# Kernel tuning notes

Measured on AMD Instinct MI355X. Metric: run time of the kernel, lower is better.

The kernel has to match this reference:

```python
import jax, jax.numpy as jnp
import numpy as np

NUM_HEADS = 16


def rotate_half(x):
    half = x.shape[-1] // 2
    return jnp.concatenate((-x[..., half:], x[..., :half]), axis=-1)


def rope_tables(seq_len, head_dim, dtype=jnp.float32):
    inv_freq = 1.0 / (10000.0 ** (jnp.arange(0, head_dim, 2, dtype=jnp.float32) / head_dim))
    t = jnp.arange(seq_len, dtype=jnp.float32)
    freqs = jnp.outer(t, inv_freq)                 # [S, hd/2]
    emb = jnp.concatenate((freqs, freqs), axis=-1)  # [S, hd]
    return jnp.cos(emb).astype(dtype), jnp.sin(emb).astype(dtype)


def setup_inputs() -> dict:
    key = jax.random.key(0)
    k1, k2, k3 = jax.random.split(key, 3)
    B, S, D = 2, 2048, 1024
    x = jax.random.normal(k1, (B, S, D), dtype=jnp.float32)
    # causal lower-triangular mask, broadcast over batch/heads
    mask = jnp.tril(jnp.ones((S, S), dtype=bool))[None, None, :, :]
    w_qkv = jax.random.normal(k2, (3 * D, D), dtype=jnp.float32) * (D ** -0.5)
    w_out = jax.random.normal(k3, (D, D), dtype=jnp.float32) * (D ** -0.5)
    return {"x": x, "mask": mask, "w_qkv": w_qkv, "w_out": w_out}


def reference(x, mask, w_qkv, w_out):
    B, S, D = x.shape
    H = NUM_HEADS
    hd = D // H
    scale = hd ** -0.5

    qkv = jnp.einsum('bsd,ed->bse', x, w_qkv)          # [B, S, 3D]
    q, k, v = jnp.split(qkv, 3, axis=-1)

    def split(t):
        return t.reshape(B, S, H, hd).transpose(0, 2, 1, 3)  # [B, H, S, hd]

    q, k, v = split(q), split(k), split(v)

    cos, sin = rope_tables(S, hd, x.dtype)             # [S, hd]
    cos = cos[None, None]
    sin = sin[None, None]
    q = q * cos + rotate_half(q) * sin
    k = k * cos + rotate_half(k) * sin

    attn = jnp.einsum('bhqd,bhkd->bhqk', q, k) * scale  # [B, H, S, S]
    attn = jnp.where(mask, attn, jnp.float32(-jnp.inf).astype(attn.dtype))
    attn = jax.nn.softmax(attn, axis=-1)
    out = jnp.einsum('bhqk,bhkd->bhqd', attn, v)        # [B, H, S, hd]
    out = out.transpose(0, 2, 1, 3).reshape(B, S, D)
    return jnp.einsum('bsd,ed->bse', out, w_out)
```

## Files before the change

kernel.cpp:

```cpp
#include <hip/hip_runtime.h>
#include <hip/hip_bf16.h>

typedef __attribute__((ext_vector_type(8))) __bf16 bf16x8;
typedef __attribute__((ext_vector_type(4))) __bf16 bf16x4;
typedef __attribute__((ext_vector_type(2))) __bf16 bf16x2;
typedef __attribute__((ext_vector_type(4))) float f32x4;
typedef __attribute__((ext_vector_type(16))) float f32x16;

#define SEQ 2048
#define NH 16
#define HD 64
#define DMODEL 1024
#define BATCH 2
#define MTOT 4096
#define NCH 26

__device__ __forceinline__ void gl_lds16(const void* g, void* l) {
    __builtin_amdgcn_global_load_lds(
        (const __attribute__((address_space(1))) void*)(uintptr_t)g,
        (__attribute__((address_space(3))) void*)(uintptr_t)l,
        16, 0, 0);
}

__device__ __forceinline__ unsigned pk2(float x, float y) {
    union { bf16x2 h; unsigned u; } c;
    c.h = bf16x2{ (__bf16)x, (__bf16)y };
    return c.u;
}

__constant__ int4 FCHUNK[32] = {
    {0,0,1,-1},{1,0,2,-1},{2,0,3,-1},{3,0,4,-1},{4,0,5,-1},{5,0,6,-1},
    {6,0,4,0},{6,4,7,1},{7,0,4,2},{7,4,8,3},
    {8,0,5,4},{8,5,9,5},{9,0,5,6},{9,5,10,7},
    {10,0,6,8},{10,6,11,9},
    {11,0,4,10},{11,4,8,11},{11,8,12,12},
    {12,0,5,13},{12,5,9,14},{12,9,13,15},
    {13,0,5,16},{13,5,10,17},{13,10,14,18},
    {14,0,5,19},{14,5,10,20},{14,10,15,21},
    {15,0,4,22},{15,4,8,23},{15,8,12,24},{15,12,16,25}
};

__global__ __launch_bounds__(256) void cast3(const float4* __restrict__ x,
                                             const float4* __restrict__ wq,
                                             const float4* __restrict__ wo,
                                             __bf16* __restrict__ xb,
                                             __bf16* __restrict__ wqb,
                                             __bf16* __restrict__ wob) {
    const int NX  = 1024 * 1024;
    const int NWQ = 768 * 1024;
    const int NTOT = NX + NWQ + 256 * 1024;
    int i = blockIdx.x * 256 + threadIdx.x;
    if (i >= NTOT) return;
    float4 v; __bf16* dst; int j;
    if (i < NX)            { j = i;            v = x[j];  dst = xb;  }
    else if (i < NX + NWQ) { j = i - NX;       v = wq[j]; dst = wqb; }
    else                   { j = i - NX - NWQ; v = wo[j]; dst = wob; }
    bf16x4 o = { (__bf16)v.x, (__bf16)v.y, (__bf16)v.z, (__bf16)v.w };
    *(bf16x4*)(dst + (size_t)j * 4) = o;
}

__global__ __launch_bounds__(256) void gemm_qkv(const __bf16* __restrict__ A,
                                                const __bf16* __restrict__ Bt,
                                                __bf16* __restrict__ Qp,
                                                __bf16* __restrict__ Kp,
                                                __bf16* __restrict__ Vt) {
    const int K = 1024;
    __shared__ __bf16 sA[128 * 64];
    __shared__ __bf16 sB[128 * 64];
    const int tid = threadIdx.x, lane = tid & 63, wave = tid >> 6;
    const int lrow = lane & 15, quad = lane >> 4;
    const int m0 = blockIdx.y * 128, n0 = blockIdx.x * 128;
    const int wm = wave >> 1, wn = wave & 1;

    const __bf16* ap[4]; const __bf16* bp[4]; int ldso[4];
#pragma unroll
    for (int i = 0; i < 4; ++i) {
        int r0 = i * 32 + wave * 8;
        int row = r0 + (lane >> 3);
        int cg = (lane & 7) ^ (row & 7);
        ap[i] = A + (size_t)(m0 + row) * K + cg * 8;
        bp[i] = Bt + (size_t)(n0 + row) * K + cg * 8;
        ldso[i] = r0 * 128;
    }
    int arow[4], brow[4];
#pragma unroll
    for (int i = 0; i < 4; ++i) {
        arow[i] = wm * 64 + i * 16 + lrow;
        brow[i] = wn * 64 + i * 16 + lrow;
    }

    f32x4 z = {0.f, 0.f, 0.f, 0.f};
    f32x4 acc[4][4];
#pragma unroll
    for (int i = 0; i < 4; ++i)
#pragma unroll
        for (int j = 0; j < 4; ++j) acc[i][j] = z;

    char* sAb = (char*)sA; char* sBb = (char*)sB;
    for (int k0 = 0; k0 < K; k0 += 64) {
#pragma unroll
        for (int i = 0; i < 4; ++i) gl_lds16(ap[i] + k0, sAb + ldso[i]);
#pragma unroll
        for (int i = 0; i < 4; ++i) gl_lds16(bp[i] + k0, sBb + ldso[i]);
        __syncthreads();
#pragma unroll
        for (int ks = 0; ks < 2; ++ks) {
            bf16x8 af[4], bfr[4];
#pragma unroll
            for (int i = 0; i < 4; ++i)
                af[i] = *(const bf16x8*)(sAb + arow[i] * 128 +
                                         (((ks * 4 + quad) ^ (arow[i] & 7)) << 4));
#pragma unroll
            for (int i = 0; i < 4; ++i)
                bfr[i] = *(const bf16x8*)(sBb + brow[i] * 128 +
                                          (((ks * 4 + quad) ^ (brow[i] & 7)) << 4));
#pragma unroll
            for (int i = 0; i < 4; ++i)
#pragma unroll
                for (int j = 0; j < 4; ++j)
                    acc[i][j] = __builtin_amdgcn_mfma_f32_16x16x32_bf16(
                        af[i], bfr[j], acc[i][j], 0, 0, 0);
        }
        __syncthreads();
    }

    const int nt = blockIdx.x;
    const int sec = nt >> 3;
    const int b = m0 >> 11;
    const int s0b = m0 & (SEQ - 1);
    const int h = (nt & 7) * 2 + wn;
    const int bh = b * NH + h;

    if (sec < 2) {
        const float scale = sec ? 1.0f : 0.18033688011112042f;
        __bf16* dst = sec ? Kp : Qp;
        float invf0 = 0.15915494309189535f *
                      exp2f(-(float)lrow * 0.4152410118609203f);
        float invf1 = invf0 * 0.01f;
#pragma unroll
        for (int i = 0; i < 4; ++i) {
            int srow0 = s0b + wm * 64 + i * 16 + quad * 4;
#pragma unroll
            for (int j = 0; j < 2; ++j) {
                float invf = j ? invf1 : invf0;
#pragma unroll
                for (int r = 0; r < 4; ++r) {
                    int s = srow0 + r;
                    float rev = (float)s * invf;
                    float fr = rev - floorf(rev);
                    float sn = __builtin_amdgcn_sinf(fr);
                    float cs = __builtin_amdgcn_cosf(fr);
                    float lo = acc[i][j][r], hi = acc[i][j + 2][r];
                    float olo = (lo * cs - hi * sn) * scale;
                    float ohi = (hi * cs + lo * sn) * scale;
                    size_t base = ((size_t)bh * SEQ + s) * HD + j * 16 + lrow;
                    dst[base] = (__bf16)olo;
                    dst[base + 32] = (__bf16)ohi;
                }
            }
        }
    } else {
#pragma unroll
        for (int i = 0; i < 4; ++i) {
            int srow0 = s0b + wm * 64 + i * 16 + quad * 4;
#pragma unroll
            for (int j = 0; j < 4; ++j) {
                int ch = j * 16 + lrow;
                bf16x4 wv = { (__bf16)acc[i][j][0], (__bf16)acc[i][j][1],
                              (__bf16)acc[i][j][2], (__bf16)acc[i][j][3] };
                *(bf16x4*)(Vt + ((size_t)bh * HD + ch) * SEQ + srow0) = wv;
            }
        }
    }
}

__global__ __launch_bounds__(256) void gemm_bt(const __bf16* __restrict__ A,
                                               const __bf16* __restrict__ Bt,
                                               float* __restrict__ Cf,
                                               int M, int N, int K) {
    __shared__ __bf16 sA[128 * 64];
    __shared__ __bf16 sB[128 * 64];
    const int tid = threadIdx.x, lane = tid & 63, wave = tid >> 6;
    const int lrow = lane & 15, quad = lane >> 4;
    const int m0 = blockIdx.y * 128, n0 = blockIdx.x * 128;
    const int wm = wave >> 1, wn = wave & 1;

    const __bf16* ap[4]; const __bf16* bp[4]; int ldso[4];
#pragma unroll
    for (int i = 0; i < 4; ++i) {
        int r0 = i * 32 + wave * 8;
        int row = r0 + (lane >> 3);
        int cg = (lane & 7) ^ (row & 7);
        ap[i] = A + (size_t)(m0 + row) * K + cg * 8;
        bp[i] = Bt + (size_t)(n0 + row) * K + cg * 8;
        ldso[i] = r0 * 128;
    }
    int arow[4], brow[4];
#pragma unroll
    for (int i = 0; i < 4; ++i) {
        arow[i] = wm * 64 + i * 16 + lrow;
        brow[i] = wn * 64 + i * 16 + lrow;
    }

    f32x4 z = {0.f, 0.f, 0.f, 0.f};
    f32x4 acc[4][4];
#pragma unroll
    for (int i = 0; i < 4; ++i)
#pragma unroll
        for (int j = 0; j < 4; ++j) acc[i][j] = z;

    char* sAb = (char*)sA; char* sBb = (char*)sB;
    for (int k0 = 0; k0 < K; k0 += 64) {
#pragma unroll
        for (int i = 0; i < 4; ++i) gl_lds16(ap[i] + k0, sAb + ldso[i]);
#pragma unroll
        for (int i = 0; i < 4; ++i) gl_lds16(bp[i] + k0, sBb + ldso[i]);
        __syncthreads();
#pragma unroll
        for (int ks = 0; ks < 2; ++ks) {
            bf16x8 af[4], bfr[4];
#pragma unroll
            for (int i = 0; i < 4; ++i)
                af[i] = *(const bf16x8*)(sAb + arow[i] * 128 +
                                         (((ks * 4 + quad) ^ (arow[i] & 7)) << 4));
#pragma unroll
            for (int i = 0; i < 4; ++i)
                bfr[i] = *(const bf16x8*)(sBb + brow[i] * 128 +
                                          (((ks * 4 + quad) ^ (brow[i] & 7)) << 4));
#pragma unroll
            for (int i = 0; i < 4; ++i)
#pragma unroll
                for (int j = 0; j < 4; ++j)
                    acc[i][j] = __builtin_amdgcn_mfma_f32_16x16x32_bf16(
                        af[i], bfr[j], acc[i][j], 0, 0, 0);
        }
        __syncthreads();
    }
#pragma unroll
    for (int i = 0; i < 4; ++i)
#pragma unroll
        for (int j = 0; j < 4; ++j)
#pragma unroll
            for (int r = 0; r < 4; ++r) {
                int row = m0 + wm * 64 + i * 16 + quad * 4 + r;
                int col = n0 + wn * 64 + j * 16 + lrow;
                Cf[(size_t)row * N + col] = acc[i][j][r];
            }
}

__global__ __launch_bounds__(256) void flash_attn(const __bf16* __restrict__ Qp,
                                                  const __bf16* __restrict__ Kp,
                                                  const __bf16* __restrict__ Vtp,
                                                  __bf16* __restrict__ Aout,
                                                  __bf16* __restrict__ Opart,
                                                  float* __restrict__ Lpart) {
    __shared__ __bf16 sK[128 * 64];
    __shared__ __bf16 sV[2][64 * 64];

    const int tid = threadIdx.x, lane = tid & 63, wave = tid >> 6;
    const int ql = lane & 31, half = lane >> 5;
    const int bh = blockIdx.x;
    const int4 chd = FCHUNK[blockIdx.y];
    const int qt = chd.x, kt0 = chd.y, kt1 = chd.z, cs = chd.w;

    const int b = bh >> 4, hh = bh & 15;
    const int q0 = qt * 128;
    const int qrow = q0 + wave * 32 + ql;

    bf16x8 qf[4];
    const __bf16* qb = Qp + ((size_t)bh * SEQ + qrow) * HD + half * 8;
#pragma unroll
    for (int kc = 0; kc < 4; ++kc) qf[kc] = *(const bf16x8*)(qb + kc * 16);

    const __bf16* kp[4]; int kldso[4];
    const __bf16* vp[4]; int vldso[4];
#pragma unroll
    for (int i = 0; i < 4; ++i) {
        int r0 = i * 32 + wave * 8;
        int row = r0 + (lane >> 3);
        int cg = (lane & 7) ^ (row & 7);
        kp[i] = Kp + ((size_t)bh * SEQ + row) * HD + cg * 8;
        kldso[i] = r0 * 128;
        int s = i >> 1;
        int rv0 = (i & 1) * 32 + wave * 8;
        int vrow = rv0 + (lane >> 3);
        int vcg = (lane & 7) ^ (vrow & 7);
        vp[i] = Vtp + ((size_t)bh * HD + vrow) * SEQ + s * 64 + vcg * 8;
        vldso[i] = s * 8192 + rv0 * 128;
    }

    char* sKb = (char*)sK;
    char* sVb = (char*)sV;

    f32x16 zz = {0.f};
    f32x16 o0 = zz, o1 = zz;
    float l = 0.f;

    for (int kt = kt0; kt < kt1; ++kt) {
        const int k0 = kt * 128;
#pragma unroll
        for (int i = 0; i < 4; ++i) gl_lds16(kp[i] + (size_t)k0 * HD, sKb + kldso[i]);
#pragma unroll
        for (int i = 0; i < 4; ++i) gl_lds16(vp[i] + k0, sVb + vldso[i]);
        __syncthreads();

        const bool diag = (kt == qt);
#pragma unroll
        for (int ktl = 0; ktl < 4; ++ktl) {
            int keyl = ktl * 32 + ql;
            f32x16 st = zz;
#pragma unroll
            for (int kc = 0; kc < 4; ++kc) {
                bf16x8 kf = *(const bf16x8*)(
                    sKb + keyl * 128 + (((kc * 2 + half) ^ (keyl & 7)) << 4));
                st = __builtin_amdgcn_mfma_f32_32x32x16_bf16(kf, qf[kc], st, 0, 0, 0);
            }

#pragma unroll
            for (int i = 0; i < 16; ++i) st[i] = exp2f(st[i]);
            if (diag) {
                int kbase = k0 + ktl * 32 + 4 * half;
#pragma unroll
                for (int g = 0; g < 4; ++g)
#pragma unroll
                    for (int t = 0; t < 4; ++t)
                        if (kbase + 8 * g + t > qrow) st[g * 4 + t] = 0.f;
            }
#pragma unroll
            for (int i = 0; i < 16; ++i) l += st[i];

#pragma unroll
            for (int lo = 0; lo < 2; ++lo) {
                union { unsigned u[4]; bf16x8 v; } pf;
#pragma unroll
                for (int d = 0; d < 4; ++d)
                    pf.u[d] = pk2(st[lo * 8 + 2 * d], st[lo * 8 + 2 * d + 1]);

                int kb = ktl * 2 + lo;
                int sv = (kb >> 2) * 8192;
                int c0 = (kb & 3) * 2, c1 = c0 + 1;
                union { bf16x4 h[2]; bf16x8 v; } vf0, vf1;
                int r0b = ql * 128, r1b = (32 + ql) * 128;
                int x0 = ((c0 ^ (ql & 7)) << 4) + 8 * half;
                int x1 = ((c1 ^ (ql & 7)) << 4) + 8 * half;
                vf0.h[0] = *(const bf16x4*)(sVb + sv + r0b + x0);
                vf0.h[1] = *(const bf16x4*)(sVb + sv + r0b + x1);
                vf1.h[0] = *(const bf16x4*)(sVb + sv + r1b + x0);
                vf1.h[1] = *(const bf16x4*)(sVb + sv + r1b + x1);
                o0 = __builtin_amdgcn_mfma_f32_32x32x16_bf16(vf0.v, pf.v, o0, 0, 0, 0);
                o1 = __builtin_amdgcn_mfma_f32_32x32x16_bf16(vf1.v, pf.v, o1, 0, 0, 0);
            }
        }
        __syncthreads();
    }

    l += __shfl_xor(l, 32, 64);
    if (cs < 0) {
        float invl = 1.0f / l;
        __bf16* obase = Aout + ((size_t)b * SEQ + qrow) * DMODEL + hh * HD;
#pragma unroll
        for (int g = 0; g < 4; ++g) {
            bf16x4 w0 = { (__bf16)(o0[g*4+0]*invl), (__bf16)(o0[g*4+1]*invl),
                          (__bf16)(o0[g*4+2]*invl), (__bf16)(o0[g*4+3]*invl) };
            bf16x4 w1 = { (__bf16)(o1[g*4+0]*invl), (__bf16)(o1[g*4+1]*invl),
                          (__bf16)(o1[g*4+2]*invl), (__bf16)(o1[g*4+3]*invl) };
            *(bf16x4*)(obase + 8 * g + 4 * half) = w0;
            *(bf16x4*)(obase + 32 + 8 * g + 4 * half) = w1;
        }
    } else {
        __bf16* ob = Opart + ((size_t)(bh * NCH + cs) << 13) +
                     (wave * 32 + ql) * 64;
#pragma unroll
        for (int g = 0; g < 4; ++g) {
            bf16x4 w0 = { (__bf16)o0[g*4+0], (__bf16)o0[g*4+1],
                          (__bf16)o0[g*4+2], (__bf16)o0[g*4+3] };
            bf16x4 w1 = { (__bf16)o1[g*4+0], (__bf16)o1[g*4+1],
                          (__bf16)o1[g*4+2], (__bf16)o1[g*4+3] };
            *(bf16x4*)(ob + 8 * g + 4 * half) = w0;
            *(bf16x4*)(ob + 32 + 8 * g + 4 * half) = w1;
        }
        if (!half)
            Lpart[(bh * NCH + cs) * 128 + wave * 32 + ql] = l;
    }
}

__global__ __launch_bounds__(256) void combine(const __bf16* __restrict__ Opart,
                                               const float* __restrict__ Lpart,
                                               __bf16* __restrict__ Aout) {
    const int bh = blockIdx.x, qy = blockIdx.y;
    const int qt = 6 + qy;
    const int Ct[10] = {2,2,2,2,2,3,3,3,3,4};
    const int cb[10] = {0,2,4,6,8,10,13,16,19,22};
    const int C = Ct[qy], cbase = cb[qy];
    const int t = threadIdx.x;
    const int row = t >> 1, hcol = (t & 1) * 32;
    float acc[32];
#pragma unroll
    for (int i = 0; i < 32; ++i) acc[i] = 0.f;
    float l = 0.f;
    for (int ci = 0; ci < C; ++ci) {
        int ch = bh * NCH + cbase + ci;
        l += Lpart[ch * 128 + row];
        const __bf16* p = Opart + ((size_t)ch << 13) + row * 64 + hcol;
#pragma unroll
        for (int k4 = 0; k4 < 4; ++k4) {
            bf16x8 v = ((const bf16x8*)p)[k4];
#pragma unroll
            for (int j = 0; j < 8; ++j) acc[k4 * 8 + j] += (float)v[j];
        }
    }
    float invl = 1.0f / l;
    const int b = bh >> 4, hh = bh & 15;
    __bf16* dst = Aout + ((size_t)(b * SEQ + qt * 128 + row)) * DMODEL +
                  hh * 64 + hcol;
#pragma unroll
    for (int k4 = 0; k4 < 4; ++k4) {
        bf16x8 w;
#pragma unroll
        for (int j = 0; j < 8; ++j) w[j] = (__bf16)(acc[k4 * 8 + j] * invl);
        ((bf16x8*)dst)[k4] = w;
    }
}

extern "C" void kernel_launch(void* const* d_in, const int* in_sizes, int n_in,
                              void* d_out, int out_size, void* d_ws, size_t ws_size,
                              hipStream_t stream) {
    (void)in_sizes; (void)n_in; (void)out_size; (void)ws_size;
    const float* x  = (const float*)d_in[0];
    const float* wq = (const float*)d_in[2];
    const float* wo = (const float*)d_in[3];
    float* out = (float*)d_out;

    char* w = (char*)d_ws;
    __bf16* xb   = (__bf16*)(w);
    __bf16* wqb  = (__bf16*)(w + (8ull << 20));
    __bf16* wob  = (__bf16*)(w + (14ull << 20));
    __bf16* Opart= (__bf16*)(w + (16ull << 20));
    float*  Lpart= (float*) (w + (35ull << 20));
    __bf16* Qb   = (__bf16*)(w + (40ull << 20));
    __bf16* Kb   = (__bf16*)(w + (48ull << 20));
    __bf16* Vtb  = (__bf16*)(w + (56ull << 20));
    __bf16* aob  = xb;

    cast3<<<8192, 256, 0, stream>>>((const float4*)x, (const float4*)wq,
                                    (const float4*)wo, xb, wqb, wob);
    gemm_qkv<<<dim3(24, 32), 256, 0, stream>>>(xb, wqb, Qb, Kb, Vtb);
    flash_attn<<<dim3(32, 32), 256, 0, stream>>>(Qb, Kb, Vtb, aob, Opart, Lpart);
    combine<<<dim3(32, 10), 256, 0, stream>>>(Opart, Lpart, aob);
    gemm_bt<<<dim3(8, 32), 256, 0, stream>>>(aob, wob, out, MTOT, 1024, 1024);
}
```

Measured before the change: 201.6 us.

## Pre-swizzle K/V into MFMA fragment layout and use single-wave split-KV attention

The QKV GEMM epilogue now writes K and V in a blocked layout that matches the MFMA operand fragments. The attention kernel can then load them straight from global memory into registers, with no LDS staging or barriers. Attention becomes a 64-thread, one-wave kernel that handles 64 query rows against 32-key tiles, using a new 80-item work table with finer split-KV chunks and heaviest items scheduled first. The combine kernel is reworked to match the new 64-row slots. This is meant to cut LDS traffic and synchronisation and to balance load across the causal triangle. The cost is more global-memory and L2 traffic, since K/V are no longer shared across waves through LDS.

```diff
diff --git a/kernel.cpp b/kernel.cpp
--- a/kernel.cpp
+++ b/kernel.cpp
@@ -13,7 +13,7 @@
 #define DMODEL 1024
 #define BATCH 2
 #define MTOT 4096
-#define NCH 26
+#define NSLOT 72
 
 __device__ __forceinline__ void gl_lds16(const void* g, void* l) {
     __builtin_amdgcn_global_load_lds(
@@ -28,16 +28,45 @@
     return c.u;
 }
 
-__constant__ int4 FCHUNK[32] = {
-    {0,0,1,-1},{1,0,2,-1},{2,0,3,-1},{3,0,4,-1},{4,0,5,-1},{5,0,6,-1},
-    {6,0,4,0},{6,4,7,1},{7,0,4,2},{7,4,8,3},
-    {8,0,5,4},{8,5,9,5},{9,0,5,6},{9,5,10,7},
-    {10,0,6,8},{10,6,11,9},
-    {11,0,4,10},{11,4,8,11},{11,8,12,12},
-    {12,0,5,13},{12,5,9,14},{12,9,13,15},
-    {13,0,5,16},{13,5,10,17},{13,10,14,18},
-    {14,0,5,19},{14,5,10,20},{14,10,15,21},
-    {15,0,4,22},{15,4,8,23},{15,8,12,24},{15,12,16,25}
+__constant__ int4 FITEM[80] = {
+    {31,0,16,68},{31,16,32,69},{31,32,48,70},{31,48,64,71},
+    {23,0,16,37},{23,16,32,38},{23,32,48,39},
+    {15,0,16,14},{15,16,32,15},
+    {30,15,31,65},{30,46,62,67},
+    {22,30,46,36},
+    {7,0,16,-1},
+    {29,0,15,60},{29,15,30,61},{29,30,45,62},{29,45,60,63},
+    {30,0,15,64},{30,31,46,66},
+    {22,0,15,34},{22,15,30,35},
+    {21,14,29,32},{21,29,44,33},
+    {28,14,29,57},{28,43,58,59},
+    {14,0,15,12},{14,15,30,13},
+    {27,0,14,52},{27,14,28,53},{27,28,42,54},{27,42,56,55},
+    {28,0,14,56},{28,29,43,58},
+    {20,0,14,28},{20,14,28,29},{20,28,42,30},
+    {21,0,14,31},
+    {26,13,27,49},{26,40,54,51},
+    {19,26,40,27},
+    {13,0,14,10},{13,14,28,11},
+    {6,0,14,-1},
+    {25,0,13,44},{25,13,26,45},{25,26,39,46},{25,39,52,47},
+    {26,0,13,48},{26,27,40,50},
+    {24,12,25,41},{24,37,50,43},
+    {19,0,13,25},{19,13,26,26},
+    {18,12,25,23},{18,25,38,24},
+    {12,0,13,8},{12,13,26,9},
+    {24,0,12,40},{24,25,37,42},
+    {17,0,12,19},{17,12,24,20},{17,24,36,21},
+    {18,0,12,22},
+    {16,22,34,18},
+    {11,0,12,6},{11,12,24,7},
+    {5,0,12,-1},
+    {16,0,11,16},{16,11,22,17},
+    {10,0,11,4},{10,11,22,5},
+    {9,0,10,2},{9,10,20,3},
+    {4,0,10,-1},
+    {8,0,9,0},{8,9,18,1},
+    {3,0,8,-1},{2,0,6,-1},{1,0,4,-1},{0,0,2,-1}
 };
 
 __global__ __launch_bounds__(256) void cast3(const float4* __restrict__ x,
@@ -62,8 +91,8 @@
 __global__ __launch_bounds__(256) void gemm_qkv(const __bf16* __restrict__ A,
                                                 const __bf16* __restrict__ Bt,
                                                 __bf16* __restrict__ Qp,
-                                                __bf16* __restrict__ Kp,
-                                                __bf16* __restrict__ Vt) {
+                                                char* __restrict__ K2,
+                                                char* __restrict__ V2) {
     const int K = 1024;
     __shared__ __bf16 sA[128 * 64];
     __shared__ __bf16 sB[128 * 64];
@@ -133,7 +162,7 @@
 
     if (sec < 2) {
         const float scale = sec ? 1.0f : 0.18033688011112042f;
-        __bf16* dst = sec ? Kp : Qp;
+        char* Kb = K2 + (size_t)bh * 262144;
         float invf0 = 0.15915494309189535f *
                       exp2f(-(float)lrow * 0.4152410118609203f);
         float invf1 = invf0 * 0.01f;
@@ -143,6 +172,7 @@
 #pragma unroll
             for (int j = 0; j < 2; ++j) {
                 float invf = j ? invf1 : invf0;
+                int hdlo = j * 16 + lrow;
 #pragma unroll
                 for (int r = 0; r < 4; ++r) {
                     int s = srow0 + r;
@@ -153,22 +183,32 @@
                     float lo = acc[i][j][r], hi = acc[i][j + 2][r];
                     float olo = (lo * cs - hi * sn) * scale;
                     float ohi = (hi * cs + lo * sn) * scale;
-                    size_t base = ((size_t)bh * SEQ + s) * HD + j * 16 + lrow;
-                    dst[base] = (__bf16)olo;
-                    dst[base + 32] = (__bf16)ohi;
+                    if (sec == 0) {
+                        size_t base = ((size_t)bh * SEQ + s) * HD + hdlo;
+                        Qp[base] = (__bf16)olo;
+                        Qp[base + 32] = (__bf16)ohi;
+                    } else {
+                        char* kt = Kb + (s >> 5) * 4096 + (s & 31) * 16 +
+                                   ((lrow >> 3) & 1) * 512 + (lrow & 7) * 2;
+                        *(__bf16*)(kt + j * 1024) = (__bf16)olo;
+                        *(__bf16*)(kt + (j + 2) * 1024) = (__bf16)ohi;
+                    }
                 }
             }
         }
     } else {
+        char* Vb = V2 + (size_t)bh * 262144;
 #pragma unroll
         for (int i = 0; i < 4; ++i) {
             int srow0 = s0b + wm * 64 + i * 16 + quad * 4;
+            int kb = srow0 >> 4, ko = srow0 & 15;
+            int slot0 = ((ko >> 2) & 1) * 8 + (ko >> 3) * 4;
 #pragma unroll
             for (int j = 0; j < 4; ++j) {
                 int ch = j * 16 + lrow;
                 bf16x4 wv = { (__bf16)acc[i][j][0], (__bf16)acc[i][j][1],
                               (__bf16)acc[i][j][2], (__bf16)acc[i][j][3] };
-                *(bf16x4*)(Vt + ((size_t)bh * HD + ch) * SEQ + srow0) = wv;
+                *(bf16x4*)(Vb + kb * 2048 + ch * 32 + slot0 * 2) = wv;
             }
         }
     }
@@ -248,177 +288,193 @@
             }
 }
 
-__global__ __launch_bounds__(256) void flash_attn(const __bf16* __restrict__ Qp,
-                                                  const __bf16* __restrict__ Kp,
-                                                  const __bf16* __restrict__ Vtp,
-                                                  __bf16* __restrict__ Aout,
-                                                  __bf16* __restrict__ Opart,
-                                                  float* __restrict__ Lpart) {
-    __shared__ __bf16 sK[128 * 64];
-    __shared__ __bf16 sV[2][64 * 64];
-
-    const int tid = threadIdx.x, lane = tid & 63, wave = tid >> 6;
+__global__ __launch_bounds__(64) void flash_attn(const __bf16* __restrict__ Qp,
+                                                 const char* __restrict__ K2,
+                                                 const char* __restrict__ V2,
+                                                 __bf16* __restrict__ Aout,
+                                                 __bf16* __restrict__ Opart,
+                                                 float* __restrict__ Lpart) {
+    const int lane = threadIdx.x;
     const int ql = lane & 31, half = lane >> 5;
     const int bh = blockIdx.x;
-    const int4 chd = FCHUNK[blockIdx.y];
-    const int qt = chd.x, kt0 = chd.y, kt1 = chd.z, cs = chd.w;
-
+    const int4 it = FITEM[blockIdx.y];
+    const int s = it.x, t0 = it.y, t1 = it.z, slot = it.w;
     const int b = bh >> 4, hh = bh & 15;
-    const int q0 = qt * 128;
-    const int qrow = q0 + wave * 32 + ql;
-
-    bf16x8 qf[4];
-    const __bf16* qb = Qp + ((size_t)bh * SEQ + qrow) * HD + half * 8;
-#pragma unroll
-    for (int kc = 0; kc < 4; ++kc) qf[kc] = *(const bf16x8*)(qb + kc * 16);
-
-    const __bf16* kp[4]; int kldso[4];
-    const __bf16* vp[4]; int vldso[4];
-#pragma unroll
-    for (int i = 0; i < 4; ++i) {
-        int r0 = i * 32 + wave * 8;
-        int row = r0 + (lane >> 3);
-        int cg = (lane & 7) ^ (row & 7);
-        kp[i] = Kp + ((size_t)bh * SEQ + row) * HD + cg * 8;
-        kldso[i] = r0 * 128;
-        int s = i >> 1;
-        int rv0 = (i & 1) * 32 + wave * 8;
-        int vrow = rv0 + (lane >> 3);
-        int vcg = (lane & 7) ^ (vrow & 7);
-        vp[i] = Vtp + ((size_t)bh * HD + vrow) * SEQ + s * 64 + vcg * 8;
-        vldso[i] = s * 8192 + rv0 * 128;
-    }
-
-    char* sKb = (char*)sK;
-    char* sVb = (char*)sV;
+
+    const __bf16* qb = Qp + ((size_t)bh * SEQ + s * 64 + ql) * HD + half * 8;
+    bf16x8 qf0[4], qf1[4];
+#pragma unroll
+    for (int kc = 0; kc < 4; ++kc) {
+        qf0[kc] = *(const bf16x8*)(qb + kc * 16);
+        qf1[kc] = *(const bf16x8*)(qb + 32 * HD + kc * 16);
+    }
+    const char* Kb = K2 + (size_t)bh * 262144 + half * 512 + ql * 16;
+    const char* Vb = V2 + (size_t)bh * 262144 + ql * 32 + half * 16;
 
     f32x16 zz = {0.f};
-    f32x16 o0 = zz, o1 = zz;
-    float l = 0.f;
-
-    for (int kt = kt0; kt < kt1; ++kt) {
-        const int k0 = kt * 128;
-#pragma unroll
-        for (int i = 0; i < 4; ++i) gl_lds16(kp[i] + (size_t)k0 * HD, sKb + kldso[i]);
-#pragma unroll
-        for (int i = 0; i < 4; ++i) gl_lds16(vp[i] + k0, sVb + vldso[i]);
-        __syncthreads();
-
-        const bool diag = (kt == qt);
-#pragma unroll
-        for (int ktl = 0; ktl < 4; ++ktl) {
-            int keyl = ktl * 32 + ql;
-            f32x16 st = zz;
-#pragma unroll
-            for (int kc = 0; kc < 4; ++kc) {
-                bf16x8 kf = *(const bf16x8*)(
-                    sKb + keyl * 128 + (((kc * 2 + half) ^ (keyl & 7)) << 4));
-                st = __builtin_amdgcn_mfma_f32_32x32x16_bf16(kf, qf[kc], st, 0, 0, 0);
+    f32x16 oA0 = zz, oA1 = zz, oB0 = zz, oB1 = zz;
+    float lA = 0.f, lB = 0.f;
+    const int dA = 2 * s, dB = 2 * s + 1;
+    const int thr = ql - 4 * half;
+
+    for (int t = t0; t < t1; ++t) {
+        bf16x8 kf[4];
+        const char* kt = Kb + t * 4096;
+#pragma unroll
+        for (int kc = 0; kc < 4; ++kc)
+            kf[kc] = *(const bf16x8*)(kt + kc * 1024);
+        bf16x8 vf[2][2];
+#pragma unroll
+        for (int lo = 0; lo < 2; ++lo) {
+            const char* vp = Vb + (t * 2 + lo) * 2048;
+            vf[lo][0] = *(const bf16x8*)(vp);
+            vf[lo][1] = *(const bf16x8*)(vp + 1024);
+        }
+        const bool do0 = (t != dB);
+
+        f32x16 st0 = zz, st1 = zz;
+        if (do0) {
+#pragma unroll
+            for (int kc = 0; kc < 4; ++kc)
+                st0 = __builtin_amdgcn_mfma_f32_32x32x16_bf16(kf[kc], qf0[kc],
+                                                              st0, 0, 0, 0);
+        }
+#pragma unroll
+        for (int kc = 0; kc < 4; ++kc)
+            st1 = __builtin_amdgcn_mfma_f32_32x32x16_bf16(kf[kc], qf1[kc],
+                                                          st1, 0, 0, 0);
+
+        if (do0) {
+#pragma unroll
+            for (int i = 0; i < 16; ++i) st0[i] = exp2f(st0[i]);
+            if (t == dA) {
+#pragma unroll
+                for (int g = 0; g < 4; ++g)
+#pragma unroll
+                    for (int tt = 0; tt < 4; ++tt)
+                        if (8 * g + tt > thr) st0[g * 4 + tt] = 0.f;
             }
-
-#pragma unroll
-            for (int i = 0; i < 16; ++i) st[i] = exp2f(st[i]);
-            if (diag) {
-                int kbase = k0 + ktl * 32 + 4 * half;
-#pragma unroll
-                for (int g = 0; g < 4; ++g)
-#pragma unroll
-                    for (int t = 0; t < 4; ++t)
-                        if (kbase + 8 * g + t > qrow) st[g * 4 + t] = 0.f;
+#pragma unroll
+            for (int i = 0; i < 16; ++i) lA += st0[i];
+        }
+#pragma unroll
+        for (int i = 0; i < 16; ++i) st1[i] = exp2f(st1[i]);
+        if (t == dB) {
+#pragma unroll
+            for (int g = 0; g < 4; ++g)
+#pragma unroll
+                for (int tt = 0; tt < 4; ++tt)
+                    if (8 * g + tt > thr) st1[g * 4 + tt] = 0.f;
+        }
+#pragma unroll
+        for (int i = 0; i < 16; ++i) lB += st1[i];
+
+#pragma unroll
+        for (int lo = 0; lo < 2; ++lo) {
+            if (do0) {
+                union { unsigned u[4]; bf16x8 v; } p0;
+#pragma unroll
+                for (int d = 0; d < 4; ++d)
+                    p0.u[d] = pk2(st0[lo * 8 + 2 * d], st0[lo * 8 + 2 * d + 1]);
+                oA0 = __builtin_amdgcn_mfma_f32_32x32x16_bf16(vf[lo][0], p0.v,
+                                                              oA0, 0, 0, 0);
+                oA1 = __builtin_amdgcn_mfma_f32_32x32x16_bf16(vf[lo][1], p0.v,
+                                                              oA1, 0, 0, 0);
             }
-#pragma unroll
-            for (int i = 0; i < 16; ++i) l += st[i];
-
-#pragma unroll
-            for (int lo = 0; lo < 2; ++lo) {
-                union { unsigned u[4]; bf16x8 v; } pf;
-#pragma unroll
-                for (int d = 0; d < 4; ++d)
-                    pf.u[d] = pk2(st[lo * 8 + 2 * d], st[lo * 8 + 2 * d + 1]);
-
-                int kb = ktl * 2 + lo;
-                int sv = (kb >> 2) * 8192;
-                int c0 = (kb & 3) * 2, c1 = c0 + 1;
-                union { bf16x4 h[2]; bf16x8 v; } vf0, vf1;
-                int r0b = ql * 128, r1b = (32 + ql) * 128;
-                int x0 = ((c0 ^ (ql & 7)) << 4) + 8 * half;
-                int x1 = ((c1 ^ (ql & 7)) << 4) + 8 * half;
-                vf0.h[0] = *(const bf16x4*)(sVb + sv + r0b + x0);
-                vf0.h[1] = *(const bf16x4*)(sVb + sv + r0b + x1);
-                vf1.h[0] = *(const bf16x4*)(sVb + sv + r1b + x0);
-                vf1.h[1] = *(const bf16x4*)(sVb + sv + r1b + x1);
-                o0 = __builtin_amdgcn_mfma_f32_32x32x16_bf16(vf0.v, pf.v, o0, 0, 0, 0);
-                o1 = __builtin_amdgcn_mfma_f32_32x32x16_bf16(vf1.v, pf.v, o1, 0, 0, 0);
-            }
-        }
-        __syncthreads();
-    }
-
-    l += __shfl_xor(l, 32, 64);
-    if (cs < 0) {
-        float invl = 1.0f / l;
-        __bf16* obase = Aout + ((size_t)b * SEQ + qrow) * DMODEL + hh * HD;
+            union { unsigned u[4]; bf16x8 v; } p1;
+#pragma unroll
+            for (int d = 0; d < 4; ++d)
+                p1.u[d] = pk2(st1[lo * 8 + 2 * d], st1[lo * 8 + 2 * d + 1]);
+            oB0 = __builtin_amdgcn_mfma_f32_32x32x16_bf16(vf[lo][0], p1.v,
+                                                          oB0, 0, 0, 0);
+            oB1 = __builtin_amdgcn_mfma_f32_32x32x16_bf16(vf[lo][1], p1.v,
+                                                          oB1, 0, 0, 0);
+        }
+    }
+
+    lA += __shfl_xor(lA, 32, 64);
+    lB += __shfl_xor(lB, 32, 64);
+
+    if (slot < 0) {
+        float iA = 1.0f / lA, iB = 1.0f / lB;
+        __bf16* oa = Aout + ((size_t)b * SEQ + s * 64 + ql) * DMODEL + hh * HD;
+        __bf16* ob = oa + (size_t)32 * DMODEL;
 #pragma unroll
         for (int g = 0; g < 4; ++g) {
-            bf16x4 w0 = { (__bf16)(o0[g*4+0]*invl), (__bf16)(o0[g*4+1]*invl),
-                          (__bf16)(o0[g*4+2]*invl), (__bf16)(o0[g*4+3]*invl) };
-            bf16x4 w1 = { (__bf16)(o1[g*4+0]*invl), (__bf16)(o1[g*4+1]*invl),
-                          (__bf16)(o1[g*4+2]*invl), (__bf16)(o1[g*4+3]*invl) };
-            *(bf16x4*)(obase + 8 * g + 4 * half) = w0;
-            *(bf16x4*)(obase + 32 + 8 * g + 4 * half) = w1;
+            bf16x4 wA0 = { (__bf16)(oA0[g*4+0]*iA), (__bf16)(oA0[g*4+1]*iA),
+                           (__bf16)(oA0[g*4+2]*iA), (__bf16)(oA0[g*4+3]*iA) };
+            bf16x4 wA1 = { (__bf16)(oA1[g*4+0]*iA), (__bf16)(oA1[g*4+1]*iA),
+                           (__bf16)(oA1[g*4+2]*iA), (__bf16)(oA1[g*4+3]*iA) };
+            bf16x4 wB0 = { (__bf16)(oB0[g*4+0]*iB), (__bf16)(oB0[g*4+1]*iB),
+                           (__bf16)(oB0[g*4+2]*iB), (__bf16)(oB0[g*4+3]*iB) };
+            bf16x4 wB1 = { (__bf16)(oB1[g*4+0]*iB), (__bf16)(oB1[g*4+1]*iB),
+                           (__bf16)(oB1[g*4+2]*iB), (__bf16)(oB1[g*4+3]*iB) };
+            *(bf16x4*)(oa + 8 * g + 4 * half) = wA0;
+            *(bf16x4*)(oa + 32 + 8 * g + 4 * half) = wA1;
+            *(bf16x4*)(ob + 8 * g + 4 * half) = wB0;
+            *(bf16x4*)(ob + 32 + 8 * g + 4 * half) = wB1;
         }
     } else {
-        __bf16* ob = Opart + ((size_t)(bh * NCH + cs) << 13) +
-                     (wave * 32 + ql) * 64;
+        __bf16* oa = Opart + ((size_t)(bh * NSLOT + slot) << 12) + ql * 64;
+        __bf16* ob = oa + 32 * 64;
 #pragma unroll
         for (int g = 0; g < 4; ++g) {
-            bf16x4 w0 = { (__bf16)o0[g*4+0], (__bf16)o0[g*4+1],
-                          (__bf16)o0[g*4+2], (__bf16)o0[g*4+3] };
-            bf16x4 w1 = { (__bf16)o1[g*4+0], (__bf16)o1[g*4+1],
-                          (__bf16)o1[g*4+2], (__bf16)o1[g*4+3] };
-            *(bf16x4*)(ob + 8 * g + 4 * half) = w0;
-            *(bf16x4*)(ob + 32 + 8 * g + 4 * half) = w1;
-        }
-        if (!half)
-            Lpart[(bh * NCH + cs) * 128 + wave * 32 + ql] = l;
+            bf16x4 wA0 = { (__bf16)oA0[g*4+0], (__bf16)oA0[g*4+1],
+                           (__bf16)oA0[g*4+2], (__bf16)oA0[g*4+3] };
+            bf16x4 wA1 = { (__bf16)oA1[g*4+0], (__bf16)oA1[g*4+1],
+                           (__bf16)oA1[g*4+2], (__bf16)oA1[g*4+3] };
+            bf16x4 wB0 = { (__bf16)oB0[g*4+0], (__bf16)oB0[g*4+1],
+                           (__bf16)oB0[g*4+2], (__bf16)oB0[g*4+3] };
+            bf16x4 wB1 = { (__bf16)oB1[g*4+0], (__bf16)oB1[g*4+1],
+                           (__bf16)oB1[g*4+2], (__bf16)oB1[g*4+3] };
+            *(bf16x4*)(oa + 8 * g + 4 * half) = wA0;
+            *(bf16x4*)(oa + 32 + 8 * g + 4 * half) = wA1;
+            *(bf16x4*)(ob + 8 * g + 4 * half) = wB0;
+            *(bf16x4*)(ob + 32 + 8 * g + 4 * half) = wB1;
+        }
+        if (!half) {
+            Lpart[(bh * NSLOT + slot) * 64 + ql] = lA;
+            Lpart[(bh * NSLOT + slot) * 64 + 32 + ql] = lB;
+        }
     }
 }
 
 __global__ __launch_bounds__(256) void combine(const __bf16* __restrict__ Opart,
                                                const float* __restrict__ Lpart,
                                                __bf16* __restrict__ Aout) {
-    const int bh = blockIdx.x, qy = blockIdx.y;
-    const int qt = 6 + qy;
-    const int Ct[10] = {2,2,2,2,2,3,3,3,3,4};
-    const int cb[10] = {0,2,4,6,8,10,13,16,19,22};
-    const int C = Ct[qy], cbase = cb[qy];
+    const int bh = blockIdx.x;
+    const int s = 8 + blockIdx.y;
+    const int C = (s < 16) ? 2 : ((s < 24) ? 3 : 4);
+    const int base = (s < 16) ? (s - 8) * 2
+                   : (s < 24) ? 16 + (s - 16) * 3
+                              : 40 + (s - 24) * 4;
     const int t = threadIdx.x;
-    const int row = t >> 1, hcol = (t & 1) * 32;
-    float acc[32];
-#pragma unroll
-    for (int i = 0; i < 32; ++i) acc[i] = 0.f;
+    const int r = t >> 2, cg = (t & 3) * 16;
+    float acc[16];
+#pragma unroll
+    for (int i = 0; i < 16; ++i) acc[i] = 0.f;
     float l = 0.f;
     for (int ci = 0; ci < C; ++ci) {
-        int ch = bh * NCH + cbase + ci;
-        l += Lpart[ch * 128 + row];
-        const __bf16* p = Opart + ((size_t)ch << 13) + row * 64 + hcol;
-#pragma unroll
-        for (int k4 = 0; k4 < 4; ++k4) {
-            bf16x8 v = ((const bf16x8*)p)[k4];
-#pragma unroll
-            for (int j = 0; j < 8; ++j) acc[k4 * 8 + j] += (float)v[j];
+        int ch = bh * NSLOT + base + ci;
+        l += Lpart[ch * 64 + r];
+        const __bf16* p = Opart + ((size_t)ch << 12) + r * 64 + cg;
+#pragma unroll
+        for (int k = 0; k < 2; ++k) {
+            bf16x8 v = ((const bf16x8*)p)[k];
+#pragma unroll
+            for (int j = 0; j < 8; ++j) acc[k * 8 + j] += (float)v[j];
         }
     }
     float invl = 1.0f / l;
     const int b = bh >> 4, hh = bh & 15;
-    __bf16* dst = Aout + ((size_t)(b * SEQ + qt * 128 + row)) * DMODEL +
-                  hh * 64 + hcol;
-#pragma unroll
-    for (int k4 = 0; k4 < 4; ++k4) {
+    __bf16* dst = Aout + ((size_t)(b * SEQ + s * 64 + r)) * DMODEL +
+                  hh * 64 + cg;
+#pragma unroll
+    for (int k = 0; k < 2; ++k) {
         bf16x8 w;
 #pragma unroll
-        for (int j = 0; j < 8; ++j) w[j] = (__bf16)(acc[k4 * 8 + j] * invl);
-        ((bf16x8*)dst)[k4] = w;
+        for (int j = 0; j < 8; ++j) w[j] = (__bf16)(acc[k * 8 + j] * invl);
+        ((bf16x8*)dst)[k] = w;
     }
 }
 
@@ -438,14 +494,14 @@
     __bf16* Opart= (__bf16*)(w + (16ull << 20));
     float*  Lpart= (float*) (w + (35ull << 20));
     __bf16* Qb   = (__bf16*)(w + (40ull << 20));
-    __bf16* Kb   = (__bf16*)(w + (48ull << 20));
-    __bf16* Vtb  = (__bf16*)(w + (56ull << 20));
+    char*   K2   = (char*)  (w + (48ull << 20));
+    char*   V2   = (char*)  (w + (56ull << 20));
     __bf16* aob  = xb;
 
     cast3<<<8192, 256, 0, stream>>>((const float4*)x, (const float4*)wq,
                                     (const float4*)wo, xb, wqb, wob);
-    gemm_qkv<<<dim3(24, 32), 256, 0, stream>>>(xb, wqb, Qb, Kb, Vtb);
-    flash_attn<<<dim3(32, 32), 256, 0, stream>>>(Qb, Kb, Vtb, aob, Opart, Lpart);
-    combine<<<dim3(32, 10), 256, 0, stream>>>(Opart, Lpart, aob);
+    gemm_qkv<<<dim3(24, 32), 256, 0, stream>>>(xb, wqb, Qb, K2, V2);
+    flash_attn<<<dim3(32, 80), 64, 0, stream>>>(Qb, K2, V2, aob, Opart, Lpart);
+    combine<<<dim3(32, 24), 256, 0, stream>>>(Opart, Lpart, aob);
     gemm_bt<<<dim3(8, 32), 256, 0, stream>>>(aob, wob, out, MTOT, 1024, 1024);
 }
```

Result: no change. 200.4 us (-0.6%).
